# Kernel optimization log

Measured on AMD Instinct MI355X. Metric: run time of the kernel, lower is better.

## Reference

```python
import jax, jax.numpy as jnp
import numpy as np

N = 100000
E = 1600000
D = 128
EPS = 1e-5


def setup_inputs() -> dict:
    key = jax.random.key(0)
    ks = jax.random.split(key, 12)
    nf_mat = jax.random.normal(ks[0], (N, D), dtype=jnp.float32)
    row = jax.random.randint(ks[1], (E,), 0, N, dtype=jnp.int32)  # target nodes
    col = jax.random.randint(ks[2], (E,), 0, N, dtype=jnp.int32)  # source nodes
    edge_weight = jax.random.uniform(ks[3], (E,), dtype=jnp.float32)
    s = 1.0 / np.sqrt(D)
    W1 = jax.random.normal(ks[4], (D, D), dtype=jnp.float32) * s
    W2 = jax.random.normal(ks[5], (D, D), dtype=jnp.float32) * s
    W3 = jax.random.normal(ks[6], (D, D), dtype=jnp.float32) * s
    b1 = jnp.zeros((D,), jnp.float32)
    b2 = jnp.zeros((D,), jnp.float32)
    b3 = jnp.zeros((D,), jnp.float32)
    gamma1 = jnp.ones((D,), jnp.float32)
    beta1 = jnp.zeros((D,), jnp.float32)
    gamma2 = jnp.ones((D,), jnp.float32)
    beta2 = jnp.zeros((D,), jnp.float32)
    # coeffs[l] = polynomial coefficients c0..c_order; init near identity (c1=1) + noise
    coeffs = jax.random.normal(ks[7], (2, 5), dtype=jnp.float32) * 0.1
    coeffs = coeffs.at[:, 1].add(1.0)
    return {"nf_mat": nf_mat, "row": row, "col": col, "edge_weight": edge_weight,
            "W1": W1, "b1": b1, "W2": W2, "b2": b2, "W3": W3, "b3": b3,
            "gamma1": gamma1, "beta1": beta1, "gamma2": gamma2, "beta2": beta2,
            "coeffs": coeffs}


def _gcn_conv(x, W, b, row, col, ew):
    # GCNConv(normalize=False): linear transform then weighted sparse aggregation
    h = x @ W                                   # [N, D]
    msg = h[col] * ew[:, None]                  # gather sources [E, D]
    agg = jax.ops.segment_sum(msg, row, num_segments=N)  # scatter to targets
    return agg + b


def _batchnorm(x, gamma, beta):
    m = jnp.mean(x, axis=0)
    v = jnp.var(x, axis=0)
    return (x - m) * jax.lax.rsqrt(v + EPS) * gamma + beta


def _poly(x, c):
    # Horner: c[0] + c[1]*x + ... + c[order]*x^order  (order=4)
    acc = jnp.full_like(x, c[-1])
    for k in range(c.shape[0] - 2, -1, -1):
        acc = acc * x + c[k]
    return acc


def reference(nf_mat, row, col, edge_weight, W1, b1, W2, b2, W3, b3,
              gamma1, beta1, gamma2, beta2, coeffs):
    x = _gcn_conv(nf_mat, W1, b1, row, col, edge_weight)
    x = _batchnorm(x, gamma1, beta1)
    x = _poly(x, coeffs[0])
    # dropout: eval mode -> identity
    x = _gcn_conv(x, W2, b2, row, col, edge_weight)
    x = _batchnorm(x, gamma2, beta2)
    x = _poly(x, coeffs[1])
    x = _gcn_conv(x, W3, b3, row, col, edge_weight)
    return x
```

## Files before the change

kernel.cpp:

```cpp
#include <hip/hip_runtime.h>
#include <hip/hip_bf16.h>

#define DD 128

typedef _Float16 h8_t __attribute__((ext_vector_type(8)));
typedef _Float16 h4_t __attribute__((ext_vector_type(4)));
typedef unsigned short us8_t __attribute__((ext_vector_type(8)));
typedef float f4_t __attribute__((ext_vector_type(4)));
typedef unsigned long long u64;

__device__ inline float bf2f(unsigned short u) {
  union { unsigned int i; float f; } v;
  v.i = ((unsigned int)u) << 16;
  return v.f;
}

__device__ inline float sat(float v) {
  return fminf(fmaxf(v, -60000.f), 60000.f);
}

__device__ inline float ldf(const void* p, int i, int f32m) {
  return f32m ? ((const float*)p)[i] : bf2f(((const unsigned short*)p)[i]);
}

#define P1_T 4096
#define NBMAX 256
#define P2_CAP 12288


__global__ __launch_bounds__(256) void k_bhist(const int* __restrict__ row,
                                               int* __restrict__ bcnt, int E, int N,
                                               const unsigned int* __restrict__ nf,
                                               int* __restrict__ flag) {
  if (blockIdx.x == gridDim.x - 1) {
    __shared__ int cnt;
    if (threadIdx.x == 0) cnt = 0;
    __syncthreads();
    int bad = 0;
#pragma unroll
    for (int k = 0; k < 8; ++k) {
      unsigned int w = nf[threadIdx.x * 8 + k];
#pragma unroll
      for (int h = 0; h < 2; ++h) {
        unsigned short us = (h == 0) ? (unsigned short)(w & 0xFFFF)
                                     : (unsigned short)(w >> 16);
        float v = bf2f(us);
        float av = fabsf(v);
        if (!(av <= 1e5f) || (av != 0.f && av < 1e-30f)) bad++;
      }
    }
    atomicAdd(&cnt, bad);
    __syncthreads();
    if (threadIdx.x == 0) *flag = (cnt > 200) ? 1 : 0;
    return;
  }
  __shared__ int hist[NBMAX];
  int tid = threadIdx.x;
  if (tid < NBMAX) hist[tid] = 0;
  __syncthreads();
  int e0 = blockIdx.x * P1_T;
#pragma unroll
  for (int k = 0; k < P1_T / 256; ++k) {
    int i = e0 + k * 256 + tid;
    if (i < E) {
      int r = row[i];
      if ((unsigned)r < (unsigned)N) atomicAdd(&hist[r >> 9], 1);
    }
  }
  __syncthreads();
  if (tid < NBMAX) {
    int c = hist[tid];
    if (c) atomicAdd(&bcnt[tid], c);
  }
}

__global__ __launch_bounds__(256) void k_bscan(const int* __restrict__ bcnt,
                                               int* __restrict__ bbase,
                                               int* __restrict__ bcur,
                                               int* __restrict__ offs,
                                               int NB, int N) {
  __shared__ int sh[NBMAX + 1];
  int tid = threadIdx.x;
  sh[tid] = (tid < NB) ? bcnt[tid] : 0;
  __syncthreads();
  if (tid == 0) {
    int run = 0;
    for (int i = 0; i < NB; ++i) {
      int t = sh[i];
      sh[i] = run;
      run += t;
    }
    sh[NB] = run;
    offs[N] = run;
  }
  __syncthreads();
  if (tid < NB) {
    bbase[tid] = sh[tid];
    bcur[tid] = sh[tid];
  }
  if (tid == 0) bbase[NB] = sh[NB];
}


__global__ __launch_bounds__(256) void k_p1(const int* __restrict__ row,
                                            const int* __restrict__ col,
                                            const void* __restrict__ ew,
                                            int* __restrict__ bcur,
                                            u64* __restrict__ stage,
                                            int E, int N, int NB,
                                            const int* __restrict__ flag) {
  __shared__ int hist[NBMAX];
  __shared__ int basep[NBMAX];
  int f32m = *flag;
  int tid = threadIdx.x;
  int e0 = blockIdx.x * P1_T;
  if (tid < NB) hist[tid] = 0;
  __syncthreads();
#pragma unroll
  for (int k = 0; k < P1_T / 256; ++k) {
    int i = e0 + k * 256 + tid;
    if (i < E) {
      int r = row[i];
      if ((unsigned)r < (unsigned)N) atomicAdd(&hist[r >> 9], 1);
    }
  }
  __syncthreads();
  if (tid < NB) {
    int c = hist[tid];
    basep[tid] = c ? atomicAdd(&bcur[tid], c) : 0;
    hist[tid] = 0;
  }
  __syncthreads();
#pragma unroll
  for (int k = 0; k < P1_T / 256; ++k) {
    int i = e0 + k * 256 + tid;
    if (i < E) {
      int r = row[i];
      if ((unsigned)r < (unsigned)N) {
        int b = r >> 9;
        int loc = atomicAdd(&hist[b], 1);
        int pos = basep[b] + loc;
        int c = col[i];
        if ((unsigned)c >= (unsigned)N) c = 0;
        unsigned int wb = __float_as_uint(ldf(ew, i, f32m));
        u64 pk = ((u64)wb << 32) | (unsigned int)(c | ((r & 511) << 17));
        stage[pos] = pk;
      }
    }
  }
}


__global__ __launch_bounds__(256) void k_p2n(const int* __restrict__ bbase,
                                             const u64* __restrict__ stage,
                                             u64* __restrict__ rec,
                                             int* __restrict__ offs, int N) {
  __shared__ int lcnt[512];
  __shared__ int lex[512];
  __shared__ int wsum[4];
  __shared__ u64 recbuf[P2_CAP];
  int b = blockIdx.x;
  int base = b << 9;
  int nend = base + 512;
  if (nend > N) nend = N;
  int nn = nend - base;
  int recbase = bbase[b];
  int cnt = bbase[b + 1] - recbase;
  int tid = threadIdx.x;
  lcnt[tid] = 0;
  lcnt[tid + 256] = 0;
  __syncthreads();
  for (int j = tid; j < cnt; j += 256) {
    unsigned int lo = (unsigned int)stage[recbase + j];
    atomicAdd(&lcnt[(lo >> 17) & 511], 1);
  }
  __syncthreads();
  int v0 = lcnt[2 * tid], v1 = lcnt[2 * tid + 1];
  int s = v0 + v1;
  int sc = s;
  int lane = tid & 63, w = tid >> 6;
#pragma unroll
  for (int d = 1; d < 64; d <<= 1) {
    int t = __shfl_up(sc, d, 64);
    if (lane >= d) sc += t;
  }
  if (lane == 63) wsum[w] = sc;
  __syncthreads();
  int wbase = 0;
  for (int x = 0; x < w; ++x) wbase += wsum[x];
  int run = wbase + (sc - s);
  lex[2 * tid] = run;
  lex[2 * tid + 1] = run + v0;
  __syncthreads();
  for (int v = tid; v < nn; v += 256) offs[base + v] = recbase + lex[v];
  lcnt[tid] = lex[tid];
  lcnt[tid + 256] = lex[tid + 256];
  __syncthreads();
  for (int j = tid; j < cnt; j += 256) {
    u64 pk = stage[recbase + j];
    unsigned int lo = (unsigned int)pk;
    unsigned int wb = (unsigned int)(pk >> 32);
    int c = lo & 0x1FFFF;
    int rloc = (lo >> 17) & 511;
    int pos = atomicAdd(&lcnt[rloc], 1);
    u64 out = ((u64)wb << 32) | (unsigned int)c;
    if (pos < P2_CAP) recbuf[pos] = out;
    else rec[recbase + pos] = out;
  }
  __syncthreads();
  int m = cnt < P2_CAP ? cnt : P2_CAP;
  for (int j = tid; j < m; j += 256) rec[recbase + j] = recbuf[j];
}


__global__ __launch_bounds__(256) void k_hist(const int* __restrict__ row,
                                              int* __restrict__ deg, int E, int N,
                                              const unsigned int* __restrict__ nf,
                                              int* __restrict__ flag) {
  if (blockIdx.x == gridDim.x - 1) {
    __shared__ int cnt;
    if (threadIdx.x == 0) cnt = 0;
    __syncthreads();
    int bad = 0;
#pragma unroll
    for (int k = 0; k < 8; ++k) {
      unsigned int w = nf[threadIdx.x * 8 + k];
#pragma unroll
      for (int h = 0; h < 2; ++h) {
        unsigned short us = (h == 0) ? (unsigned short)(w & 0xFFFF)
                                     : (unsigned short)(w >> 16);
        float v = bf2f(us);
        float av = fabsf(v);
        if (!(av <= 1e5f) || (av != 0.f && av < 1e-30f)) bad++;
      }
    }
    atomicAdd(&cnt, bad);
    __syncthreads();
    if (threadIdx.x == 0) *flag = (cnt > 200) ? 1 : 0;
    return;
  }
  int i = blockIdx.x * 256 + threadIdx.x;
  if (i < E) {
    int r = row[i];
    if ((unsigned)r < (unsigned)N) atomicAdd(&deg[r], 1);
  }
}

__global__ __launch_bounds__(256) void k_scan1(const int* __restrict__ deg,
                                               int* __restrict__ bsum, int n) {
  int i0 = blockIdx.x * 1024 + threadIdx.x * 4;
  int s = 0;
#pragma unroll
  for (int k = 0; k < 4; ++k) {
    int i = i0 + k;
    if (i < n) s += deg[i];
  }
#pragma unroll
  for (int d = 1; d < 64; d <<= 1) s += __shfl_xor(s, d, 64);
  __shared__ int ws[4];
  int lane = threadIdx.x & 63, w = threadIdx.x >> 6;
  if (lane == 0) ws[w] = s;
  __syncthreads();
  if (threadIdx.x == 0) bsum[blockIdx.x] = ws[0] + ws[1] + ws[2] + ws[3];
}

__global__ __launch_bounds__(1024) void k_scan2(int* __restrict__ bsum,
                                                int* __restrict__ offs,
                                                int nb, int n) {
  __shared__ int sh[1024];
  int tid = threadIdx.x;
  sh[tid] = (tid < nb) ? bsum[tid] : 0;
  __syncthreads();
  if (tid == 0) {
    int run = 0;
    for (int i = 0; i < nb; ++i) {
      int t = sh[i];
      sh[i] = run;
      run += t;
    }
    offs[n] = run;
  }
  __syncthreads();
  if (tid < nb) bsum[tid] = sh[tid];
}

__global__ __launch_bounds__(256) void k_scan3(const int* __restrict__ deg,
                                               const int* __restrict__ bsum,
                                               int* __restrict__ offs,
                                               int* __restrict__ cursor, int n) {
  int tid = threadIdx.x, lane = tid & 63, w = tid >> 6;
  int i0 = blockIdx.x * 1024 + tid * 4;
  int v0 = 0, v1 = 0, v2 = 0, v3 = 0;
  if (i0 + 3 < n) {
    v0 = deg[i0]; v1 = deg[i0 + 1]; v2 = deg[i0 + 2]; v3 = deg[i0 + 3];
  } else {
    if (i0 < n) v0 = deg[i0];
    if (i0 + 1 < n) v1 = deg[i0 + 1];
    if (i0 + 2 < n) v2 = deg[i0 + 2];
  }
  int s = v0 + v1 + v2 + v3;
  int sc = s;
#pragma unroll
  for (int d = 1; d < 64; d <<= 1) {
    int t = __shfl_up(sc, d, 64);
    if (lane >= d) sc += t;
  }
  __shared__ int ws[4];
  if (lane == 63) ws[w] = sc;
  __syncthreads();
  int wbase = 0;
  for (int x = 0; x < w; ++x) wbase += ws[x];
  int run = bsum[blockIdx.x] + wbase + (sc - s);
  if (i0 < n)     { offs[i0] = run;     cursor[i0] = run;     run += v0; }
  if (i0 + 1 < n) { offs[i0 + 1] = run; cursor[i0 + 1] = run; run += v1; }
  if (i0 + 2 < n) { offs[i0 + 2] = run; cursor[i0 + 2] = run; run += v2; }
  if (i0 + 3 < n) { offs[i0 + 3] = run; cursor[i0 + 3] = run; }
}

__global__ __launch_bounds__(256) void k_fill(const int* __restrict__ row,
                                              const int* __restrict__ col,
                                              const void* __restrict__ ew,
                                              int* __restrict__ cursor,
                                              int2* __restrict__ rec, int E, int N,
                                              const int* __restrict__ flag) {
  int f32m = *flag;
  int i = blockIdx.x * 256 + threadIdx.x;
  if (i >= E) return;
  int r = row[i];
  if ((unsigned)r >= (unsigned)N) return;
  int p = atomicAdd(&cursor[r], 1);
  if ((unsigned)p >= (unsigned)E) return;
  int c = col[i];
  if ((unsigned)c >= (unsigned)N) c = 0;
  rec[p] = make_int2(c, __float_as_int(ldf(ew, i, f32m)));
}

__global__ __launch_bounds__(256) void k_cvt_w(const void* __restrict__ W1,
                                               const void* __restrict__ W2,
                                               const void* __restrict__ W3,
                                               _Float16* __restrict__ Wt,
                                               const int* __restrict__ flag) {
  int f32m = *flag;
  int i = blockIdx.x * 256 + threadIdx.x;
  if (i >= 3 * 16384) return;
  int l = i >> 14, o = i & 16383;
  int j = o & 7, lane = (o >> 3) & 63, kkt = o >> 9;
  int kk = kkt & 3, t = kkt >> 2;
  int k = kk * 32 + (lane >> 4) * 8 + j;
  int n = t * 16 + (lane & 15);
  const void* W = (l == 0) ? W1 : (l == 1 ? W2 : W3);
  Wt[i] = (_Float16)ldf(W, k * 128 + n, f32m);
}


__global__ __launch_bounds__(128) void k_bnprep(const float* __restrict__ pb,
                                                const void* __restrict__ gamma,
                                                const void* __restrict__ beta,
                                                const void* __restrict__ coeffs,
                                                int coff, float invN,
                                                float* __restrict__ bn,
                                                const int* __restrict__ flag) {
  int f32m = *flag;
  int c = threadIdx.x;
  float s = 0.f, s2 = 0.f;
#pragma unroll 8
  for (int p = 0; p < 64; ++p) {
    s += pb[p * 256 + c];
    s2 += pb[p * 256 + 128 + c];
  }
  float mn = s * invN;
  float var = fmaf(-mn, mn, s2 * invN);
  var = fmaxf(var, 0.0f);
  float inv = rsqrtf(var + 1e-5f);
  float g = ldf(gamma, c, f32m);
  float scv = g * inv;
  bn[c] = scv;
  bn[128 + c] = ldf(beta, c, f32m) - mn * scv;
  if (c < 5) bn[256 + c] = ldf(coeffs, coff + c, f32m);
}


template <int MODE>
__global__ __launch_bounds__(256) void k_gemm(const void* __restrict__ Xraw,
                                              const _Float16* __restrict__ Wt,
                                              _Float16* __restrict__ H, int nrows,
                                              const float* __restrict__ bn,
                                              const int* __restrict__ flag,
                                              float* __restrict__ pbz) {
  if (pbz != nullptr && blockIdx.x < 64)
    pbz[(blockIdx.x << 8) + threadIdx.x] = 0.f;
  int gw = (blockIdx.x * 256 + threadIdx.x) >> 6;
  int lane = threadIdx.x & 63;
  int r0 = gw << 4;
  if (r0 >= nrows) return;
  int m = lane & 15, q = lane >> 4;
  int rr = r0 + m;
  if (rr >= nrows) rr = nrows - 1;
  h8_t a[4];
  if (MODE == 0) {
    int f32m = *flag;
    if (f32m) {
      const float* X = (const float*)Xraw + (size_t)rr * DD + q * 8;
#pragma unroll
      for (int kk = 0; kk < 4; ++kk) {
        float4 u0 = *(const float4*)(X + kk * 32);
        float4 u1 = *(const float4*)(X + kk * 32 + 4);
        a[kk] = h8_t{(_Float16)u0.x, (_Float16)u0.y, (_Float16)u0.z, (_Float16)u0.w,
                     (_Float16)u1.x, (_Float16)u1.y, (_Float16)u1.z, (_Float16)u1.w};
      }
    } else {
      const unsigned short* X = (const unsigned short*)Xraw + (size_t)rr * DD + q * 8;
#pragma unroll
      for (int kk = 0; kk < 4; ++kk) {
        us8_t u = *(const us8_t*)(X + kk * 32);
        h8_t o;
#pragma unroll
        for (int j = 0; j < 8; ++j) o[j] = (_Float16)bf2f(u[j]);
        a[kk] = o;
      }
    }
  } else {
    const _Float16* X = (const _Float16*)Xraw + (size_t)rr * DD + q * 8;
    const float* scp = bn;
    const float* shp = bn + 128;
    float p0 = bn[256], p1 = bn[257], p2 = bn[258], p3 = bn[259], p4 = bn[260];
#pragma unroll
    for (int kk = 0; kk < 4; ++kk) {
      h8_t x = *(const h8_t*)(X + kk * 32);
      int c0 = kk * 32 + q * 8;
      float scv[8], shv[8];
      *(float4*)scv = *(const float4*)(scp + c0);
      *(float4*)(scv + 4) = *(const float4*)(scp + c0 + 4);
      *(float4*)shv = *(const float4*)(shp + c0);
      *(float4*)(shv + 4) = *(const float4*)(shp + c0 + 4);
      h8_t o;
#pragma unroll
      for (int j = 0; j < 8; ++j) {
        float xn = fmaf((float)x[j], scv[j], shv[j]);
        xn = fminf(fmaxf(xn, -100.f), 100.f);
        float h = p4;
        h = fmaf(h, xn, p3);
        h = fmaf(h, xn, p2);
        h = fmaf(h, xn, p1);
        h = fmaf(h, xn, p0);
        o[j] = (_Float16)h;
      }
      a[kk] = o;
    }
  }
  f4_t acc[8] = {};
#pragma unroll
  for (int kk = 0; kk < 4; ++kk) {
#pragma unroll
    for (int t = 0; t < 8; ++t) {
      h8_t b = *(const h8_t*)(Wt + (((t * 4 + kk) * 64 + lane) << 3));
      acc[t] = __builtin_amdgcn_mfma_f32_16x16x32_f16(a[kk], b, acc[t], 0, 0, 0);
    }
  }
#pragma unroll
  for (int t = 0; t < 8; ++t) {
#pragma unroll
    for (int r = 0; r < 4; ++r) {
      int orow = r0 + q * 4 + r;
      if (orow < nrows)
        H[(size_t)orow * DD + t * 16 + m] = (_Float16)sat(acc[t][r]);
    }
  }
}


template <int FINAL, int STATS>
__global__ __launch_bounds__(256) void k_agg(const _Float16* __restrict__ h,
                                             const int* __restrict__ offs,
                                             const int2* __restrict__ rec,
                                             const void* __restrict__ bias,
                                             void* __restrict__ outp, int n, int E,
                                             const int* __restrict__ flag,
                                             float* __restrict__ pb) {
  int f32m = *flag;
  int wid = threadIdx.x >> 6;
  int lane = threadIdx.x & 63;
  int sub = lane >> 4;
  int fl = lane & 15;
  const uint4* h128 = (const uint4*)h;
  float ss[8] = {}, ss2[8] = {};
  float bv[8];
  {
    int c0 = fl << 3;
#pragma unroll
    for (int k = 0; k < 8; ++k) bv[k] = ldf(bias, c0 + k, f32m);
  }
#pragma unroll 1
  for (int t = 0; t < 4; ++t) {
    int node = (blockIdx.x << 4) + (wid << 2) + t;
    bool act = node < n;
    int beg = 0, end = 0;
    if (act) {
      beg = offs[node];
      end = offs[node + 1];
      if (beg < 0) beg = 0;
      if (end > E) end = E;
    }
    float a8[8] = {};
    for (int base = beg; base < end; base += 64) {
      int mm = end - base;
      if (mm > 64) mm = 64;
      int c = 0, wb = 0;
      if (lane < mm) {
        int2 r = rec[base + lane];
        c = r.x;
        wb = r.y;
      }
#pragma unroll 4
      for (int j = 0; j < mm; j += 4) {
        int idx = j + sub;
        int cc = __shfl(c, idx);
        float ww = __int_as_float(__shfl(wb, idx));
        if ((unsigned)cc >= (unsigned)n) cc = 0;
        union { uint4 u; h8_t f; } cv;
        cv.u = h128[(size_t)cc * 16 + fl];
#pragma unroll
        for (int k = 0; k < 8; ++k) a8[k] = fmaf((float)cv.f[k], ww, a8[k]);
      }
    }
#pragma unroll
    for (int k = 0; k < 8; ++k) a8[k] += __shfl_xor(a8[k], 16);
#pragma unroll
    for (int k = 0; k < 8; ++k) a8[k] += __shfl_xor(a8[k], 32);
    if (lane < 16 && act) {
      float o[8];
#pragma unroll
      for (int k = 0; k < 8; ++k) o[k] = sat(a8[k] + bv[k]);
      if (FINAL) {
        float4 v0 = make_float4(o[0], o[1], o[2], o[3]);
        float4 v1 = make_float4(o[4], o[5], o[6], o[7]);
        ((float4*)outp)[(size_t)node * 32 + fl * 2] = v0;
        ((float4*)outp)[(size_t)node * 32 + fl * 2 + 1] = v1;
      } else {
        union { uint4 u; h8_t f; } cv;
#pragma unroll
        for (int k = 0; k < 8; ++k) cv.f[k] = (_Float16)o[k];
        ((uint4*)outp)[(size_t)node * 16 + fl] = cv.u;
      }
      if (STATS) {
#pragma unroll
        for (int k = 0; k < 8; ++k) {
          ss[k] += o[k];
          ss2[k] = fmaf(o[k], o[k], ss2[k]);
        }
      }
    }
  }
  if (STATS) {
    __shared__ float sh[4][256];
    if (lane < 16) {
      int c0 = fl << 3;
#pragma unroll
      for (int k = 0; k < 8; ++k) {
        sh[wid][c0 + k] = ss[k];
        sh[wid][128 + c0 + k] = ss2[k];
      }
    }
    __syncthreads();
    int tid = threadIdx.x;
    float v = sh[0][tid] + sh[1][tid] + sh[2][tid] + sh[3][tid];
    float* dst = pb + ((blockIdx.x & 63) << 8);
    atomicAdd(&dst[tid], v);
  }
}


extern "C" void kernel_launch(void* const* d_in, const int* in_sizes, int n_in,
                              void* d_out, int out_size, void* d_ws, size_t ws_size,
                              hipStream_t stream) {
  const void* nf = d_in[0];
  const int* row = (const int*)d_in[1];
  const int* col = (const int*)d_in[2];
  const void* ew = d_in[3];
  const void* W1 = d_in[4];
  const void* b1 = d_in[5];
  const void* W2 = d_in[6];
  const void* b2 = d_in[7];
  const void* W3 = d_in[8];
  const void* b3 = d_in[9];
  const void* g1 = d_in[10];
  const void* be1 = d_in[11];
  const void* g2 = d_in[12];
  const void* be2 = d_in[13];
  const void* coeffs = d_in[14];

  const int N = in_sizes[0] / DD;
  const int E = in_sizes[1];
  const int cstride = in_sizes[14] / 2;

  char* p = (char*)d_ws;
  auto alloc = [&](size_t bytes) {
    char* r = p;
    p += (bytes + 255) & ~(size_t)255;
    return r;
  };
  int* flag = (int*)alloc(256);
  float* bn = (float*)alloc(2048);
  float* pb = (float*)alloc(65536);
  int* bsum = (int*)alloc(4096);
  int* bcnt = (int*)alloc(1024);
  int* bbase = (int*)alloc(1088);
  int* bcur = (int*)alloc(1024);
  _Float16* Wt = (_Float16*)alloc(3 * 16384 * 2);
  _Float16* H16 = (_Float16*)alloc((size_t)N * DD * 2);
  int* deg = (int*)alloc((size_t)N * 4);
  int* offs = (int*)alloc((size_t)(N + 1) * 4);
  int* cursor = (int*)alloc((size_t)N * 4);
  int2* rec = (int2*)alloc((size_t)E * 8);
  u64* stage = (u64*)alloc((size_t)E * 8);

  _Float16* OUT = (_Float16*)d_out;

  int NB = (N + 511) >> 9;
  int p1b = (E + P1_T - 1) / P1_T;
  if (NB <= NBMAX) {
    hipMemsetAsync(bcnt, 0, 1024, stream);
    k_bhist<<<p1b + 1, 256, 0, stream>>>(row, bcnt, E, N, (const unsigned int*)nf, flag);
    k_bscan<<<1, 256, 0, stream>>>(bcnt, bbase, bcur, offs, NB, N);
    k_p1<<<p1b, 256, 0, stream>>>(row, col, ew, bcur, stage, E, N, NB, flag);
    k_p2n<<<NB, 256, 0, stream>>>(bbase, stage, (u64*)rec, offs, N);
  } else {
    int eb = (E + 255) / 256;
    hipMemsetAsync(deg, 0, (size_t)N * 4, stream);
    k_hist<<<eb + 1, 256, 0, stream>>>(row, deg, E, N, (const unsigned int*)nf, flag);
    int nb = (N + 1023) / 1024;
    k_scan1<<<nb, 256, 0, stream>>>(deg, bsum, N);
    k_scan2<<<1, 1024, 0, stream>>>(bsum, offs, nb, N);
    k_scan3<<<nb, 256, 0, stream>>>(deg, bsum, offs, cursor, N);
    k_fill<<<eb, 256, 0, stream>>>(row, col, ew, cursor, rec, E, N, flag);
  }

  k_cvt_w<<<192, 256, 0, stream>>>(W1, W2, W3, Wt, flag);

  int gemm_blocks = ((N + 15) / 16 + 3) / 4;
  int agg_blocks = (N + 15) / 16;
  float invN = 1.0f / (float)N;

  const void* Bs[3] = {b1, b2, b3};
  const void* Gs[2] = {g1, g2};
  const void* Bes[2] = {be1, be2};

  k_gemm<0><<<gemm_blocks, 256, 0, stream>>>(nf, Wt, H16, N, bn, flag, pb);
  k_agg<0, 1><<<agg_blocks, 256, 0, stream>>>(H16, offs, rec, Bs[0], OUT, N, E, flag, pb);
  k_bnprep<<<1, 128, 0, stream>>>(pb, Gs[0], Bes[0], coeffs, 0, invN, bn, flag);

  k_gemm<1><<<gemm_blocks, 256, 0, stream>>>(OUT, Wt + 16384, H16, N, bn, flag, pb);
  k_agg<0, 1><<<agg_blocks, 256, 0, stream>>>(H16, offs, rec, Bs[1], OUT, N, E, flag, pb);
  k_bnprep<<<1, 128, 0, stream>>>(pb, Gs[1], Bes[1], coeffs, cstride, invN, bn, flag);

  k_gemm<1><<<gemm_blocks, 256, 0, stream>>>(OUT, Wt + 2 * 16384, H16, N, bn, flag, nullptr);
  k_agg<1, 0><<<agg_blocks, 256, 0, stream>>>(H16, offs, rec, Bs[2], d_out, N, E, flag, pb);
}
```

Before: 501.6 us.

## Fuse BN-prep into aggregation tail, reuse block histograms, merge weight conversion

After: 1.725 ms. 3.44x slower.

```diff
diff --git a/kernel.cpp b/kernel.cpp
--- a/kernel.cpp
+++ b/kernel.cpp
@@ -27,11 +27,26 @@
 #define NBMAX 256
 #define P2_CAP 12288
 
+__device__ inline void cvt_w_body(const void* __restrict__ W1,
+                                  const void* __restrict__ W2,
+                                  const void* __restrict__ W3,
+                                  _Float16* __restrict__ Wt, int f32m, int i) {
+  if (i >= 3 * 16384) return;
+  int l = i >> 14, o = i & 16383;
+  int j = o & 7, lane = (o >> 3) & 63, kkt = o >> 9;
+  int kk = kkt & 3, t = kkt >> 2;
+  int k = kk * 32 + (lane >> 4) * 8 + j;
+  int n = t * 16 + (lane & 15);
+  const void* W = (l == 0) ? W1 : (l == 1 ? W2 : W3);
+  Wt[i] = (_Float16)ldf(W, k * 128 + n, f32m);
+}
+
 
 __global__ __launch_bounds__(256) void k_bhist(const int* __restrict__ row,
                                                int* __restrict__ bcnt, int E, int N,
                                                const unsigned int* __restrict__ nf,
-                                               int* __restrict__ flag) {
+                                               int* __restrict__ flag,
+                                               int* __restrict__ blkhist) {
   if (blockIdx.x == gridDim.x - 1) {
     __shared__ int cnt;
     if (threadIdx.x == 0) cnt = 0;
@@ -56,7 +71,7 @@
   }
   __shared__ int hist[NBMAX];
   int tid = threadIdx.x;
-  if (tid < NBMAX) hist[tid] = 0;
+  hist[tid] = 0;
   __syncthreads();
   int e0 = blockIdx.x * P1_T;
 #pragma unroll
@@ -68,10 +83,9 @@
     }
   }
   __syncthreads();
-  if (tid < NBMAX) {
-    int c = hist[tid];
-    if (c) atomicAdd(&bcnt[tid], c);
-  }
+  int c = hist[tid];
+  blkhist[blockIdx.x * 256 + tid] = c;
+  if (c) atomicAdd(&bcnt[tid], c);
 }
 
 __global__ __launch_bounds__(256) void k_bscan(const int* __restrict__ bcnt,
@@ -108,25 +122,23 @@
                                             int* __restrict__ bcur,
                                             u64* __restrict__ stage,
                                             int E, int N, int NB,
-                                            const int* __restrict__ flag) {
+                                            const int* __restrict__ flag,
+                                            const int* __restrict__ blkhist,
+                                            const void* __restrict__ W1,
+                                            const void* __restrict__ W2,
+                                            const void* __restrict__ W3,
+                                            _Float16* __restrict__ Wt, int p1b) {
+  int f32m = *flag;
+  if (blockIdx.x >= p1b) {
+    cvt_w_body(W1, W2, W3, Wt, f32m, (blockIdx.x - p1b) * 256 + threadIdx.x);
+    return;
+  }
   __shared__ int hist[NBMAX];
   __shared__ int basep[NBMAX];
-  int f32m = *flag;
   int tid = threadIdx.x;
   int e0 = blockIdx.x * P1_T;
-  if (tid < NB) hist[tid] = 0;
-  __syncthreads();
-#pragma unroll
-  for (int k = 0; k < P1_T / 256; ++k) {
-    int i = e0 + k * 256 + tid;
-    if (i < E) {
-      int r = row[i];
-      if ((unsigned)r < (unsigned)N) atomicAdd(&hist[r >> 9], 1);
-    }
-  }
-  __syncthreads();
   if (tid < NB) {
-    int c = hist[tid];
+    int c = blkhist[blockIdx.x * 256 + tid];
     basep[tid] = c ? atomicAdd(&bcur[tid], c) : 0;
     hist[tid] = 0;
   }
@@ -340,43 +352,7 @@
                                                const void* __restrict__ W3,
                                                _Float16* __restrict__ Wt,
                                                const int* __restrict__ flag) {
-  int f32m = *flag;
-  int i = blockIdx.x * 256 + threadIdx.x;
-  if (i >= 3 * 16384) return;
-  int l = i >> 14, o = i & 16383;
-  int j = o & 7, lane = (o >> 3) & 63, kkt = o >> 9;
-  int kk = kkt & 3, t = kkt >> 2;
-  int k = kk * 32 + (lane >> 4) * 8 + j;
-  int n = t * 16 + (lane & 15);
-  const void* W = (l == 0) ? W1 : (l == 1 ? W2 : W3);
-  Wt[i] = (_Float16)ldf(W, k * 128 + n, f32m);
-}
-
-
-__global__ __launch_bounds__(128) void k_bnprep(const float* __restrict__ pb,
-                                                const void* __restrict__ gamma,
-                                                const void* __restrict__ beta,
-                                                const void* __restrict__ coeffs,
-                                                int coff, float invN,
-                                                float* __restrict__ bn,
-                                                const int* __restrict__ flag) {
-  int f32m = *flag;
-  int c = threadIdx.x;
-  float s = 0.f, s2 = 0.f;
-#pragma unroll 8
-  for (int p = 0; p < 64; ++p) {
-    s += pb[p * 256 + c];
-    s2 += pb[p * 256 + 128 + c];
-  }
-  float mn = s * invN;
-  float var = fmaf(-mn, mn, s2 * invN);
-  var = fmaxf(var, 0.0f);
-  float inv = rsqrtf(var + 1e-5f);
-  float g = ldf(gamma, c, f32m);
-  float scv = g * inv;
-  bn[c] = scv;
-  bn[128 + c] = ldf(beta, c, f32m) - mn * scv;
-  if (c < 5) bn[256 + c] = ldf(coeffs, coff + c, f32m);
+  cvt_w_body(W1, W2, W3, Wt, *flag, blockIdx.x * 256 + threadIdx.x);
 }
 
 
@@ -386,9 +362,11 @@
                                               _Float16* __restrict__ H, int nrows,
                                               const float* __restrict__ bn,
                                               const int* __restrict__ flag,
-                                              float* __restrict__ pbz) {
+                                              float* __restrict__ pbz,
+                                              int* __restrict__ ctrz) {
   if (pbz != nullptr && blockIdx.x < 64)
     pbz[(blockIdx.x << 8) + threadIdx.x] = 0.f;
+  if (ctrz != nullptr && blockIdx.x == 0 && threadIdx.x == 0) *ctrz = 0;
   int gw = (blockIdx.x * 256 + threadIdx.x) >> 6;
   int lane = threadIdx.x & 63;
   int r0 = gw << 4;
@@ -476,7 +454,13 @@
                                              const void* __restrict__ bias,
                                              void* __restrict__ outp, int n, int E,
                                              const int* __restrict__ flag,
-                                             float* __restrict__ pb) {
+                                             float* __restrict__ pb,
+                                             int* __restrict__ ctr,
+                                             const void* __restrict__ gamma,
+                                             const void* __restrict__ beta,
+                                             const void* __restrict__ coeffs,
+                                             int coff, float invN,
+                                             float* __restrict__ bn) {
   int f32m = *flag;
   int wid = threadIdx.x >> 6;
   int lane = threadIdx.x & 63;
@@ -566,6 +550,31 @@
     float v = sh[0][tid] + sh[1][tid] + sh[2][tid] + sh[3][tid];
     float* dst = pb + ((blockIdx.x & 63) << 8);
     atomicAdd(&dst[tid], v);
+    __threadfence();
+    __shared__ int lastFlag;
+    if (tid == 0) lastFlag = (atomicAdd(ctr, 1) == (int)gridDim.x - 1);
+    __syncthreads();
+    if (lastFlag) {
+      __threadfence();
+      if (tid < 128) {
+        int c = tid;
+        float s = 0.f, s2 = 0.f;
+#pragma unroll 8
+        for (int p = 0; p < 64; ++p) {
+          s += pb[p * 256 + c];
+          s2 += pb[p * 256 + 128 + c];
+        }
+        float mn = s * invN;
+        float var = fmaf(-mn, mn, s2 * invN);
+        var = fmaxf(var, 0.0f);
+        float inv = rsqrtf(var + 1e-5f);
+        float g = ldf(gamma, c, f32m);
+        float scv = g * inv;
+        bn[c] = scv;
+        bn[128 + c] = ldf(beta, c, f32m) - mn * scv;
+        if (c < 5) bn[256 + c] = ldf(coeffs, coff + c, f32m);
+      }
+    }
   }
 }
 
@@ -602,10 +611,13 @@
   int* flag = (int*)alloc(256);
   float* bn = (float*)alloc(2048);
   float* pb = (float*)alloc(65536);
+  int* ctr = (int*)alloc(256);
   int* bsum = (int*)alloc(4096);
   int* bcnt = (int*)alloc(1024);
   int* bbase = (int*)alloc(1088);
   int* bcur = (int*)alloc(1024);
+  int p1b = (E + P1_T - 1) / P1_T;
+  int* blkhist = (int*)alloc((size_t)p1b * 256 * 4);
   _Float16* Wt = (_Float16*)alloc(3 * 16384 * 2);
   _Float16* H16 = (_Float16*)alloc((size_t)N * DD * 2);
   int* deg = (int*)alloc((size_t)N * 4);
@@ -617,12 +629,13 @@
   _Float16* OUT = (_Float16*)d_out;
 
   int NB = (N + 511) >> 9;
-  int p1b = (E + P1_T - 1) / P1_T;
   if (NB <= NBMAX) {
     hipMemsetAsync(bcnt, 0, 1024, stream);
-    k_bhist<<<p1b + 1, 256, 0, stream>>>(row, bcnt, E, N, (const unsigned int*)nf, flag);
+    k_bhist<<<p1b + 1, 256, 0, stream>>>(row, bcnt, E, N, (const unsigned int*)nf,
+                                         flag, blkhist);
     k_bscan<<<1, 256, 0, stream>>>(bcnt, bbase, bcur, offs, NB, N);
-    k_p1<<<p1b, 256, 0, stream>>>(row, col, ew, bcur, stage, E, N, NB, flag);
+    k_p1<<<p1b + 192, 256, 0, stream>>>(row, col, ew, bcur, stage, E, N, NB, flag,
+                                        blkhist, W1, W2, W3, Wt, p1b);
     k_p2n<<<NB, 256, 0, stream>>>(bbase, stage, (u64*)rec, offs, N);
   } else {
     int eb = (E + 255) / 256;
@@ -633,26 +646,26 @@
     k_scan2<<<1, 1024, 0, stream>>>(bsum, offs, nb, N);
     k_scan3<<<nb, 256, 0, stream>>>(deg, bsum, offs, cursor, N);
     k_fill<<<eb, 256, 0, stream>>>(row, col, ew, cursor, rec, E, N, flag);
-  }
-
-  k_cvt_w<<<192, 256, 0, stream>>>(W1, W2, W3, Wt, flag);
+    k_cvt_w<<<192, 256, 0, stream>>>(W1, W2, W3, Wt, flag);
+  }
 
   int gemm_blocks = ((N + 15) / 16 + 3) / 4;
   int agg_blocks = (N + 15) / 16;
   float invN = 1.0f / (float)N;
 
-  const void* Bs[3] = {b1, b2, b3};
-  const void* Gs[2] = {g1, g2};
-  const void* Bes[2] = {be1, be2};
-
-  k_gemm<0><<<gemm_blocks, 256, 0, stream>>>(nf, Wt, H16, N, bn, flag, pb);
-  k_agg<0, 1><<<agg_blocks, 256, 0, stream>>>(H16, offs, rec, Bs[0], OUT, N, E, flag, pb);
-  k_bnprep<<<1, 128, 0, stream>>>(pb, Gs[0], Bes[0], coeffs, 0, invN, bn, flag);
-
-  k_gemm<1><<<gemm_blocks, 256, 0, stream>>>(OUT, Wt + 16384, H16, N, bn, flag, pb);
-  k_agg<0, 1><<<agg_blocks, 256, 0, stream>>>(H16, offs, rec, Bs[1], OUT, N, E, flag, pb);
-  k_bnprep<<<1, 128, 0, stream>>>(pb, Gs[1], Bes[1], coeffs, cstride, invN, bn, flag);
-
-  k_gemm<1><<<gemm_blocks, 256, 0, stream>>>(OUT, Wt + 2 * 16384, H16, N, bn, flag, nullptr);
-  k_agg<1, 0><<<agg_blocks, 256, 0, stream>>>(H16, offs, rec, Bs[2], d_out, N, E, flag, pb);
-}
+  k_gemm<0><<<gemm_blocks, 256, 0, stream>>>(nf, Wt, H16, N, bn, flag, pb, ctr);
+  k_agg<0, 1><<<agg_blocks, 256, 0, stream>>>(H16, offs, rec, b1, OUT, N, E, flag,
+                                              pb, ctr, g1, be1, coeffs, 0, invN, bn);
+
+  k_gemm<1><<<gemm_blocks, 256, 0, stream>>>(OUT, Wt + 16384, H16, N, bn, flag,
+                                             pb, ctr + 1);
+  k_agg<0, 1><<<agg_blocks, 256, 0, stream>>>(H16, offs, rec, b2, OUT, N, E, flag,
+                                              pb, ctr + 1, g2, be2, coeffs, cstride,
+                                              invN, bn);
+
+  k_gemm<1><<<gemm_blocks, 256, 0, stream>>>(OUT, Wt + 2 * 16384, H16, N, bn, flag,
+                                             nullptr, nullptr);
+  k_agg<1, 0><<<agg_blocks, 256, 0, stream>>>(H16, offs, rec, b3, d_out, N, E, flag,
+                                              pb, nullptr, nullptr, nullptr, nullptr,
+                                              0, invN, bn);
+}
```
